# Kernel optimization log

Hardware: AMD Instinct MI355X
Metric: run time of the kernel (lower is better)

## Reference

```python
import jax, jax.numpy as jnp
import numpy as np

NUM_HEADS = 8
NUM_GROUPS = 8
EPS = 1e-5

def group_norm(x, scale, bias):
    b, c, h, w = x.shape
    xg = x.reshape(b, NUM_GROUPS, c // NUM_GROUPS, h, w)
    mean = xg.mean(axis=(2, 3, 4), keepdims=True)
    var = xg.var(axis=(2, 3, 4), keepdims=True)
    xn = ((xg - mean) / jnp.sqrt(var + EPS)).reshape(b, c, h, w)
    return xn * scale[None, :, None, None] + bias[None, :, None, None]

def setup_inputs() -> dict:
    key = jax.random.key(0)
    ks = jax.random.split(key, 7)
    C = 512
    x = jax.random.normal(ks[0], (16, C, 32, 32), dtype=jnp.float32)
    gn_scale = jnp.ones((C,), jnp.float32)
    gn_bias = jnp.zeros((C,), jnp.float32)
    w_qkv = jax.random.normal(ks[1], (3 * C, C), dtype=jnp.float32) * (1.0 / np.sqrt(C))
    b_qkv = jax.random.normal(ks[2], (3 * C,), dtype=jnp.float32) * 0.01
    w_proj = jax.random.normal(ks[3], (C, C), dtype=jnp.float32) * (1.0 / np.sqrt(C))
    b_proj = jax.random.normal(ks[4], (C,), dtype=jnp.float32) * 0.01
    return {"x": x, "gn_scale": gn_scale, "gn_bias": gn_bias,
            "w_qkv": w_qkv, "b_qkv": b_qkv, "w_proj": w_proj, "b_proj": b_proj}

def reference(x, gn_scale, gn_bias, w_qkv, b_qkv, w_proj, b_proj):
    b, c, h, w = x.shape
    hd = c // NUM_HEADS
    hn = group_norm(x, gn_scale, gn_bias)
    # 1x1 conv == per-pixel linear: [b,3c,h,w]
    qkv = jnp.einsum('oc,bchw->bohw', w_qkv, hn) + b_qkv[None, :, None, None]
    q, k, v = jnp.split(qkv, 3, axis=1)
    # -> [b, heads, seq, head_dim], seq = h*w
    def to_heads(t):
        return t.reshape(b, NUM_HEADS, hd, h * w).transpose(0, 1, 3, 2)
    q, k, v = to_heads(q), to_heads(k), to_heads(v)
    scale = 1.0 / jnp.sqrt(jnp.asarray(hd, x.dtype))
    attn = jnp.einsum('bnqd,bnkd->bnqk', q, k) * scale
    attn = jax.nn.softmax(attn, axis=-1)
    out = jnp.einsum('bnqk,bnkd->bnqd', attn, v)
    out = out.transpose(0, 1, 3, 2).reshape(b, c, h, w)
    out = jnp.einsum('oc,bchw->bohw', w_proj, out) + b_proj[None, :, None, None]
    return x + out
```

## Files before the change

### kernel.cpp

```cpp
#include <hip/hip_runtime.h>

typedef _Float16 half8 __attribute__((ext_vector_type(8)));
typedef _Float16 half4 __attribute__((ext_vector_type(4)));
typedef float f32x4 __attribute__((ext_vector_type(4)));

__device__ inline unsigned short f2h(float f) {
  union { _Float16 h; unsigned short u; } cv;
  cv.h = (_Float16)f;
  return cv.u;
}

__device__ inline unsigned int pk2(float a, float b) {
  return __builtin_bit_cast(unsigned int, __builtin_amdgcn_cvt_pkrtz(a, b));
}

__device__ inline void gload_lds16(const void* g, void* l) {
  __builtin_amdgcn_global_load_lds(
      (const __attribute__((address_space(1))) void*)g,
      (__attribute__((address_space(3))) void*)l, 16, 0, 0);
}

__global__ __launch_bounds__(256) void prep(const float* __restrict__ wqkv,
                                            const float* __restrict__ wproj,
                                            _Float16* __restrict__ wq,
                                            _Float16* __restrict__ wp,
                                            const float* __restrict__ x,
                                            float* __restrict__ mr) {
  if (blockIdx.x < 3072) {
    const int i = blockIdx.x * 256 + threadIdx.x;
    wq[i] = (_Float16)wqkv[i];
    if (i < 262144) wp[i] = (_Float16)wproj[i];
    return;
  }
  const int sb = blockIdx.x - 3072;
  const float4* xv = (const float4*)(x + (size_t)sb * 32768);
  float s = 0.f, s2 = 0.f;
  for (int i = threadIdx.x; i < 8192; i += 256) {
    float4 v = xv[i];
    s += v.x + v.y + v.z + v.w;
    s2 += v.x * v.x + v.y * v.y + v.z * v.z + v.w * v.w;
  }
  for (int m = 32; m; m >>= 1) {
    s += __shfl_down(s, m);
    s2 += __shfl_down(s2, m);
  }
  __shared__ float ls[4], ls2[4];
  const int wid = threadIdx.x >> 6;
  if ((threadIdx.x & 63) == 0) { ls[wid] = s; ls2[wid] = s2; }
  __syncthreads();
  if (threadIdx.x == 0) {
    mr[sb * 2] = ls[0] + ls[1] + ls[2] + ls[3];
    mr[sb * 2 + 1] = ls2[0] + ls2[1] + ls2[2] + ls2[3];
  }
}

__global__ __launch_bounds__(256) void gn_apply(const float* __restrict__ x,
                                                const float* __restrict__ mr,
                                                const float* __restrict__ sc,
                                                const float* __restrict__ bi,
                                                _Float16* __restrict__ hn) {
  __shared__ __align__(16) _Float16 t[64][72];
  const int b = blockIdx.z, cb = blockIdx.y, pb = blockIdx.x;
  const int c0 = cb * 64, p0 = pb * 64;
  const int bg = b * 8 + cb;
  const float S = mr[bg * 4 + 0] + mr[bg * 4 + 2];
  const float S2 = mr[bg * 4 + 1] + mr[bg * 4 + 3];
  const float mean = S * (1.f / 65536.f);
  const float var = S2 * (1.f / 65536.f) - mean * mean;
  const float rstd = rsqrtf(var + 1e-5f);
  const int tp = threadIdx.x & 63;
  const int tc = threadIdx.x >> 6;
#pragma unroll
  for (int i = 0; i < 16; i++) {
    const int c = tc * 16 + i;
    const float g = sc[c0 + c] * rstd;
    const float v = x[((size_t)b * 512 + c0 + c) * 1024 + p0 + tp];
    t[tp][c] = (_Float16)((v - mean) * g + bi[c0 + c]);
  }
  __syncthreads();
  const int wp = threadIdx.x >> 2;
  const int wc = (threadIdx.x & 3) * 16;
  _Float16* dst = hn + ((size_t)b * 1024 + p0 + wp) * 512 + c0 + wc;
  *(uint4*)dst = *(const uint4*)&t[wp][wc];
  *(uint4*)(dst + 8) = *(const uint4*)&t[wp][wc + 8];
}

template <int EPI>
__global__ __launch_bounds__(256) void gemm_mfma(
    const _Float16* __restrict__ A, const _Float16* __restrict__ Bt,
    const float* __restrict__ bias, const float* __restrict__ xin,
    float* __restrict__ fout, _Float16* __restrict__ qo,
    _Float16* __restrict__ ko, _Float16* __restrict__ vo) {
  __shared__ __align__(16) _Float16 As[128 * 64];
  __shared__ __align__(16) _Float16 Bs[128 * 64];
  const int b = blockIdx.z;
  const int m0 = blockIdx.y * 128, n0 = blockIdx.x * 128;
  const char* Ab = (const char*)A;
  const char* Bb = (const char*)(Bt + (size_t)b * 1024 * 512);
  const int t = threadIdx.x, lane = t & 63, w = t >> 6;
  const int wm = (w >> 1) * 64, wn = (w & 1) * 64;
  const int lr = lane & 15, lk = lane >> 4;
  int srow[4], scb[4];
#pragma unroll
  for (int it = 0; it < 4; it++) {
    srow[it] = it * 32 + w * 8 + (lane >> 3);
    scb[it] = ((lane & 7) * 16) ^ ((srow[it] & 7) << 4);
  }
  f32x4 acc[4][4] = {};
#pragma unroll 1
  for (int k0 = 0; k0 < 512; k0 += 64) {
#pragma unroll
    for (int it = 0; it < 4; it++) {
      const size_t go = (size_t)(m0 + srow[it]) * 1024 + k0 * 2 + scb[it];
      const size_t gob = (size_t)(n0 + srow[it]) * 1024 + k0 * 2 + scb[it];
      char* la = (char*)As + it * 4096 + w * 1024;
      char* lb = (char*)Bs + it * 4096 + w * 1024;
      gload_lds16(Ab + go, la);
      gload_lds16(Bb + gob, lb);
    }
    __syncthreads();
#pragma unroll
    for (int kk = 0; kk < 2; kk++) {
      half8 af[4], bf[4];
#pragma unroll
      for (int i = 0; i < 4; i++) {
        const int ra = wm + i * 16 + lr;
        af[i] = *(const half8*)((const char*)As +
                                ((ra * 128 + kk * 64 + lk * 16) ^ ((ra & 7) << 4)));
        const int rb = wn + i * 16 + lr;
        bf[i] = *(const half8*)((const char*)Bs +
                                ((rb * 128 + kk * 64 + lk * 16) ^ ((rb & 7) << 4)));
      }
#pragma unroll
      for (int i = 0; i < 4; i++)
#pragma unroll
        for (int j = 0; j < 4; j++)
          acc[i][j] = __builtin_amdgcn_mfma_f32_16x16x32_f16(af[i], bf[j],
                                                             acc[i][j], 0, 0, 0);
    }
    __syncthreads();
  }
#pragma unroll
  for (int i = 0; i < 4; i++) {
    const int o = m0 + wm + i * 16 + lk * 4;
#pragma unroll
    for (int j = 0; j < 4; j++) {
      const int p = n0 + wn + j * 16 + lr;
      float vv[4];
#pragma unroll
      for (int r = 0; r < 4; r++) vv[r] = acc[i][j][r] + bias[o + r];
      if (EPI == 0) {
        const int sec = o >> 9, oc = o & 511;
        const int h = oc >> 6, d0 = oc & 63;
        if (sec == 0) {
          const float qs = 0.125f * 1.44269504f;
          ushort4 pk;
          pk.x = f2h(vv[0] * qs); pk.y = f2h(vv[1] * qs);
          pk.z = f2h(vv[2] * qs); pk.w = f2h(vv[3] * qs);
          *(ushort4*)(qo + ((size_t)(b * 8 + h) * 1024 + p) * 64 + d0) = pk;
        } else if (sec == 1) {
          ushort4 pk;
          pk.x = f2h(vv[0]); pk.y = f2h(vv[1]);
          pk.z = f2h(vv[2]); pk.w = f2h(vv[3]);
          *(ushort4*)(ko + ((size_t)(b * 8 + h) * 1024 + p) * 64 + d0) = pk;
        } else {
#pragma unroll
          for (int r = 0; r < 4; r++)
            vo[((size_t)(b * 8 + h) * 64 + d0 + r) * 1024 + p] = (_Float16)vv[r];
        }
      } else {
        const size_t idx = ((size_t)b * 512 + o) * 1024 + p;
#pragma unroll
        for (int r = 0; r < 4; r++)
          fout[idx + (size_t)r * 1024] = xin[idx + (size_t)r * 1024] + vv[r];
      }
    }
  }
}

__global__ __launch_bounds__(512, 4) void attn(const _Float16* __restrict__ q,
                                               const _Float16* __restrict__ k,
                                               const _Float16* __restrict__ v,
                                               _Float16* __restrict__ o) {
  __shared__ __align__(16) _Float16 KT[2][4096];
  __shared__ __align__(16) _Float16 VT[2][4096];
  __shared__ __align__(16) _Float16 PT[8][2048];
  const int id = blockIdx.x;
  const int flat = (id & 7) * 64 + (id >> 3);
  const int qb = flat & 3, bh = flat >> 2;
  const int b = bh >> 3, h = bh & 7;
  const int t = threadIdx.x, lane = t & 63, w = t >> 6;
  const int lr = lane & 15, lk = lane >> 4;
  const int q0 = qb * 256 + w * 32;
  const _Float16* qp = q + (size_t)bh * 65536;
  const char* kc = (const char*)(k + (size_t)bh * 65536);
  const char* vc = (const char*)(v + (size_t)bh * 65536);
  const int srow = t >> 3, scol = (t & 7) * 16;
  const int sdst = srow * 128 + (scol ^ ((srow & 7) << 4));
  int koff[4][2];
#pragma unroll
  for (int j = 0; j < 4; j++) {
    const int row = j * 16 + lr, sw = (row & 7) << 4;
    koff[j][0] = row * 128 + ((lk * 16) ^ sw);
    koff[j][1] = row * 128 + ((64 + lk * 16) ^ sw);
  }
  int pwoff[2][4];
#pragma unroll
  for (int g = 0; g < 2; g++) {
    const int qhat = g * 16 + lr, sw = (qhat & 7) << 4;
#pragma unroll
    for (int j = 0; j < 4; j++)
      pwoff[g][j] = qhat * 128 + ((j * 32 + lk * 8) ^ sw);
  }
  half8 qf[2][2];
#pragma unroll
  for (int g = 0; g < 2; g++)
#pragma unroll
    for (int kk = 0; kk < 2; kk++)
      qf[g][kk] = *(const half8*)(qp + (q0 + g * 16 + lr) * 64 + kk * 32 + lk * 8);
  const half8 onesv = {(_Float16)1.f, (_Float16)1.f, (_Float16)1.f, (_Float16)1.f,
                       (_Float16)1.f, (_Float16)1.f, (_Float16)1.f, (_Float16)1.f};
  {
    uint4 k0 = *(const uint4*)(kc + srow * 128 + scol);
    uint4 v0 = *(const uint4*)(vc + srow * 2048 + scol);
    *(uint4*)((char*)KT + sdst) = k0;
    *(uint4*)((char*)VT + sdst) = v0;
  }
  __syncthreads();
  f32x4 aco[2][4] = {};
  f32x4 lacc[2] = {};
  char* Pc = (char*)PT + w * 4096;
#pragma unroll 1
  for (int kt = 0; kt < 16; kt++) {
    const int cur = kt & 1;
    const char* Kc = (const char*)KT + cur * 8192;
    const char* Vc = (const char*)VT + cur * 8192;
    uint4 kn, vn;
    if (kt < 15) {
      kn = *(const uint4*)(kc + (kt + 1) * 8192 + srow * 128 + scol);
      vn = *(const uint4*)(vc + srow * 2048 + (kt + 1) * 128 + scol);
    }
    f32x4 s[2][4] = {};
    __builtin_amdgcn_s_setprio(1);
#pragma unroll
    for (int j = 0; j < 4; j++) {
      const half8 kf0 = *(const half8*)(Kc + koff[j][0]);
      const half8 kf1 = *(const half8*)(Kc + koff[j][1]);
#pragma unroll
      for (int g = 0; g < 2; g++) {
        s[g][j] = __builtin_amdgcn_mfma_f32_16x16x32_f16(kf0, qf[g][0], s[g][j], 0, 0, 0);
        s[g][j] = __builtin_amdgcn_mfma_f32_16x16x32_f16(kf1, qf[g][1], s[g][j], 0, 0, 0);
      }
    }
    __builtin_amdgcn_s_setprio(0);
#pragma unroll
    for (int g = 0; g < 2; g++) {
#pragma unroll
      for (int j = 0; j < 4; j++) {
        uint2 pw;
        pw.x = pk2(exp2f(s[g][j][0] - 10.f), exp2f(s[g][j][1] - 10.f));
        pw.y = pk2(exp2f(s[g][j][2] - 10.f), exp2f(s[g][j][3] - 10.f));
        *(uint2*)(Pc + pwoff[g][j]) = pw;
      }
    }
    __builtin_amdgcn_s_setprio(1);
#pragma unroll
    for (int kk = 0; kk < 2; kk++) {
      half8 vf[4];
#pragma unroll
      for (int jd = 0; jd < 4; jd++)
        vf[jd] = *(const half8*)(Vc + koff[jd][kk]);
#pragma unroll
      for (int g = 0; g < 2; g++) {
        const half8 pf = *(const half8*)(Pc + koff[g][kk]);
        lacc[g] = __builtin_amdgcn_mfma_f32_16x16x32_f16(pf, onesv, lacc[g], 0, 0, 0);
#pragma unroll
        for (int jd = 0; jd < 4; jd++)
          aco[g][jd] = __builtin_amdgcn_mfma_f32_16x16x32_f16(pf, vf[jd], aco[g][jd], 0, 0, 0);
      }
    }
    __builtin_amdgcn_s_setprio(0);
    if (kt < 15) {
      *(uint4*)((char*)KT + (cur ^ 1) * 8192 + sdst) = kn;
      *(uint4*)((char*)VT + (cur ^ 1) * 8192 + sdst) = vn;
    }
    __syncthreads();
  }
#pragma unroll
  for (int g = 0; g < 2; g++)
#pragma unroll
    for (int r = 0; r < 4; r++) {
      const float rl = 1.f / lacc[g][r];
      const int row = q0 + g * 16 + 4 * lk + r;
#pragma unroll
      for (int jd = 0; jd < 4; jd++)
        o[((size_t)b * 1024 + row) * 512 + h * 64 + jd * 16 + lr] =
            (_Float16)(aco[g][jd][r] * rl);
    }
}

extern "C" void kernel_launch(void* const* d_in, const int* in_sizes, int n_in,
                              void* d_out, int out_size, void* d_ws, size_t ws_size,
                              hipStream_t stream) {
  const float* x = (const float*)d_in[0];
  const float* gsc = (const float*)d_in[1];
  const float* gbi = (const float*)d_in[2];
  const float* wqkv = (const float*)d_in[3];
  const float* bqkv = (const float*)d_in[4];
  const float* wproj = (const float*)d_in[5];
  const float* bproj = (const float*)d_in[6];
  float* out = (float*)d_out;
  char* ws = (char*)d_ws;
  float* mr = (float*)ws;
  _Float16* wq16 = (_Float16*)(ws + 4096);
  _Float16* wp16 = (_Float16*)(ws + 4096 + 1572864);
  _Float16* hn = (_Float16*)(ws + 2101248);
  _Float16* q16 = (_Float16*)(ws + 18878464);
  _Float16* k16 = (_Float16*)(ws + 35655680);
  _Float16* v16 = (_Float16*)(ws + 52432896);

  hipLaunchKernelGGL(prep, dim3(3328), dim3(256), 0, stream, wqkv, wproj, wq16,
                     wp16, x, mr);
  hipLaunchKernelGGL(gn_apply, dim3(16, 8, 16), dim3(256), 0, stream, x, mr, gsc,
                     gbi, hn);
  hipLaunchKernelGGL((gemm_mfma<0>), dim3(8, 12, 16), dim3(256), 0, stream, wq16,
                     hn, bqkv, (const float*)nullptr, (float*)nullptr, q16, k16,
                     v16);
  hipLaunchKernelGGL(attn, dim3(512), dim3(512), 0, stream, q16, k16, v16, hn);
  hipLaunchKernelGGL((gemm_mfma<1>), dim3(8, 4, 16), dim3(256), 0, stream, wp16,
                     hn, bproj, x, out, (_Float16*)nullptr, (_Float16*)nullptr,
                     (_Float16*)nullptr);
}
```

Measured before the change: 144.1 us.

## Halve per-warp query rows in attention and write head-major output layout

The attention kernel now gives each warp 16 query rows instead of 32, doubling the grid to 1024 blocks and halving the P scratch in LDS. The launch-bounds hint is raised to allow more resident blocks. Output is written head-major, [bh][seq][64], with contiguous rows, and the projection GEMM's B-operand addressing is changed to read that layout. The aim is more parallelism and occupancy plus coalesced output stores, at the cost of reloading K/V tiles twice as often per query.

```diff
diff --git a/kernel.cpp b/kernel.cpp
--- a/kernel.cpp
+++ b/kernel.cpp
@@ -112,7 +112,11 @@
 #pragma unroll
     for (int it = 0; it < 4; it++) {
       const size_t go = (size_t)(m0 + srow[it]) * 1024 + k0 * 2 + scb[it];
-      const size_t gob = (size_t)(n0 + srow[it]) * 1024 + k0 * 2 + scb[it];
+      const size_t gob =
+          (EPI == 0)
+              ? (size_t)(n0 + srow[it]) * 1024 + k0 * 2 + scb[it]
+              : (size_t)(k0 >> 6) * 131072 + (size_t)(n0 + srow[it]) * 128 +
+                    scb[it];
       char* la = (char*)As + it * 4096 + w * 1024;
       char* lb = (char*)Bs + it * 4096 + w * 1024;
       gload_lds16(Ab + go, la);
@@ -178,20 +182,19 @@
   }
 }
 
-__global__ __launch_bounds__(512, 4) void attn(const _Float16* __restrict__ q,
+__global__ __launch_bounds__(512, 6) void attn(const _Float16* __restrict__ q,
                                                const _Float16* __restrict__ k,
                                                const _Float16* __restrict__ v,
                                                _Float16* __restrict__ o) {
   __shared__ __align__(16) _Float16 KT[2][4096];
   __shared__ __align__(16) _Float16 VT[2][4096];
-  __shared__ __align__(16) _Float16 PT[8][2048];
+  __shared__ __align__(16) _Float16 PT[8][1024];
   const int id = blockIdx.x;
-  const int flat = (id & 7) * 64 + (id >> 3);
-  const int qb = flat & 3, bh = flat >> 2;
-  const int b = bh >> 3, h = bh & 7;
+  const int flat = (id & 7) * 128 + (id >> 3);
+  const int qb = flat & 7, bh = flat >> 3;
   const int t = threadIdx.x, lane = t & 63, w = t >> 6;
   const int lr = lane & 15, lk = lane >> 4;
-  const int q0 = qb * 256 + w * 32;
+  const int q0 = qb * 128 + w * 16;
   const _Float16* qp = q + (size_t)bh * 65536;
   const char* kc = (const char*)(k + (size_t)bh * 65536);
   const char* vc = (const char*)(v + (size_t)bh * 65536);
@@ -204,20 +207,17 @@
     koff[j][0] = row * 128 + ((lk * 16) ^ sw);
     koff[j][1] = row * 128 + ((64 + lk * 16) ^ sw);
   }
-  int pwoff[2][4];
-#pragma unroll
-  for (int g = 0; g < 2; g++) {
-    const int qhat = g * 16 + lr, sw = (qhat & 7) << 4;
+  int pwoff[4];
+  {
+    const int sw = (lr & 7) << 4;
 #pragma unroll
     for (int j = 0; j < 4; j++)
-      pwoff[g][j] = qhat * 128 + ((j * 32 + lk * 8) ^ sw);
-  }
-  half8 qf[2][2];
-#pragma unroll
-  for (int g = 0; g < 2; g++)
-#pragma unroll
-    for (int kk = 0; kk < 2; kk++)
-      qf[g][kk] = *(const half8*)(qp + (q0 + g * 16 + lr) * 64 + kk * 32 + lk * 8);
+      pwoff[j] = lr * 128 + ((j * 32 + lk * 8) ^ sw);
+  }
+  half8 qf[2];
+#pragma unroll
+  for (int kk = 0; kk < 2; kk++)
+    qf[kk] = *(const half8*)(qp + (q0 + lr) * 64 + kk * 32 + lk * 8);
   const half8 onesv = {(_Float16)1.f, (_Float16)1.f, (_Float16)1.f, (_Float16)1.f,
                        (_Float16)1.f, (_Float16)1.f, (_Float16)1.f, (_Float16)1.f};
   {
@@ -227,9 +227,9 @@
     *(uint4*)((char*)VT + sdst) = v0;
   }
   __syncthreads();
-  f32x4 aco[2][4] = {};
-  f32x4 lacc[2] = {};
-  char* Pc = (char*)PT + w * 4096;
+  f32x4 aco[4] = {};
+  f32x4 lacc = {};
+  char* Pc = (char*)PT + w * 2048;
 #pragma unroll 1
   for (int kt = 0; kt < 16; kt++) {
     const int cur = kt & 1;
@@ -240,28 +240,22 @@
       kn = *(const uint4*)(kc + (kt + 1) * 8192 + srow * 128 + scol);
       vn = *(const uint4*)(vc + srow * 2048 + (kt + 1) * 128 + scol);
     }
-    f32x4 s[2][4] = {};
+    f32x4 s[4] = {};
     __builtin_amdgcn_s_setprio(1);
 #pragma unroll
     for (int j = 0; j < 4; j++) {
       const half8 kf0 = *(const half8*)(Kc + koff[j][0]);
       const half8 kf1 = *(const half8*)(Kc + koff[j][1]);
-#pragma unroll
-      for (int g = 0; g < 2; g++) {
-        s[g][j] = __builtin_amdgcn_mfma_f32_16x16x32_f16(kf0, qf[g][0], s[g][j], 0, 0, 0);
-        s[g][j] = __builtin_amdgcn_mfma_f32_16x16x32_f16(kf1, qf[g][1], s[g][j], 0, 0, 0);
-      }
+      s[j] = __builtin_amdgcn_mfma_f32_16x16x32_f16(kf0, qf[0], s[j], 0, 0, 0);
+      s[j] = __builtin_amdgcn_mfma_f32_16x16x32_f16(kf1, qf[1], s[j], 0, 0, 0);
     }
     __builtin_amdgcn_s_setprio(0);
 #pragma unroll
-    for (int g = 0; g < 2; g++) {
-#pragma unroll
-      for (int j = 0; j < 4; j++) {
-        uint2 pw;
-        pw.x = pk2(exp2f(s[g][j][0] - 10.f), exp2f(s[g][j][1] - 10.f));
-        pw.y = pk2(exp2f(s[g][j][2] - 10.f), exp2f(s[g][j][3] - 10.f));
-        *(uint2*)(Pc + pwoff[g][j]) = pw;
-      }
+    for (int j = 0; j < 4; j++) {
+      uint2 pw;
+      pw.x = pk2(exp2f(s[j][0] - 10.f), exp2f(s[j][1] - 10.f));
+      pw.y = pk2(exp2f(s[j][2] - 10.f), exp2f(s[j][3] - 10.f));
+      *(uint2*)(Pc + pwoff[j]) = pw;
     }
     __builtin_amdgcn_s_setprio(1);
 #pragma unroll
@@ -270,14 +264,11 @@
 #pragma unroll
       for (int jd = 0; jd < 4; jd++)
         vf[jd] = *(const half8*)(Vc + koff[jd][kk]);
-#pragma unroll
-      for (int g = 0; g < 2; g++) {
-        const half8 pf = *(const half8*)(Pc + koff[g][kk]);
-        lacc[g] = __builtin_amdgcn_mfma_f32_16x16x32_f16(pf, onesv, lacc[g], 0, 0, 0);
-#pragma unroll
-        for (int jd = 0; jd < 4; jd++)
-          aco[g][jd] = __builtin_amdgcn_mfma_f32_16x16x32_f16(pf, vf[jd], aco[g][jd], 0, 0, 0);
-      }
+      const half8 pf = *(const half8*)(Pc + koff[0][kk]);
+      lacc = __builtin_amdgcn_mfma_f32_16x16x32_f16(pf, onesv, lacc, 0, 0, 0);
+#pragma unroll
+      for (int jd = 0; jd < 4; jd++)
+        aco[jd] = __builtin_amdgcn_mfma_f32_16x16x32_f16(pf, vf[jd], aco[jd], 0, 0, 0);
     }
     __builtin_amdgcn_s_setprio(0);
     if (kt < 15) {
@@ -286,17 +277,15 @@
     }
     __syncthreads();
   }
-#pragma unroll
-  for (int g = 0; g < 2; g++)
-#pragma unroll
-    for (int r = 0; r < 4; r++) {
-      const float rl = 1.f / lacc[g][r];
-      const int row = q0 + g * 16 + 4 * lk + r;
-#pragma unroll
-      for (int jd = 0; jd < 4; jd++)
-        o[((size_t)b * 1024 + row) * 512 + h * 64 + jd * 16 + lr] =
-            (_Float16)(aco[g][jd][r] * rl);
-    }
+  _Float16* ob = o + (size_t)bh * 65536;
+#pragma unroll
+  for (int r = 0; r < 4; r++) {
+    const float rl = 1.f / lacc[r];
+    const int row = q0 + 4 * lk + r;
+#pragma unroll
+    for (int jd = 0; jd < 4; jd++)
+      ob[row * 64 + jd * 16 + lr] = (_Float16)(aco[jd][r] * rl);
+  }
 }
 
 extern "C" void kernel_launch(void* const* d_in, const int* in_sizes, int n_in,
@@ -326,7 +315,7 @@
   hipLaunchKernelGGL((gemm_mfma<0>), dim3(8, 12, 16), dim3(256), 0, stream, wq16,
                      hn, bqkv, (const float*)nullptr, (float*)nullptr, q16, k16,
                      v16);
-  hipLaunchKernelGGL(attn, dim3(512), dim3(512), 0, stream, q16, k16, v16, hn);
+  hipLaunchKernelGGL(attn, dim3(1024), dim3(512), 0, stream, q16, k16, v16, hn);
   hipLaunchKernelGGL((gemm_mfma<1>), dim3(8, 4, 16), dim3(256), 0, stream, wp16,
                      hn, bproj, x, out, (_Float16*)nullptr, (_Float16*)nullptr,
                      (_Float16*)nullptr);
```

Result: slower. 149.3 us (+3.6%).
